# Performance work log

Hardware: AMD Instinct MI355X
Metric: run time of the kernel (lower is better)

The kernel has to match this reference:

```python
import jax, jax.numpy as jnp
import numpy as np

B, T, D, H = 1, 4096, 1024, 16
DK = D // H
SCALE = 1.0 / float(np.sqrt(DK))
NEG = -1e9


def setup_inputs() -> dict:
    key = jax.random.key(0)
    k1, k2, k3 = jax.random.split(key, 3)
    x = jax.random.normal(k1, (B, T, D), dtype=jnp.float32)
    # xavier-ish small weights (gain 0.5)
    Wqkv = jax.random.normal(k2, (3 * D, D), dtype=jnp.float32) * 0.02
    Wout = jax.random.normal(k3, (D, D), dtype=jnp.float32) * 0.02
    return {"x": x, "Wqkv": Wqkv, "Wout": Wout}


def reference(x, Wqkv, Wout):
    b, t, d = x.shape
    # QKV projection (no bias): [B,T,3D] -> [3,B,H,T,DK]
    qkv = jnp.einsum('btd,ed->bte', x, Wqkv)
    qkv = qkv.reshape(b, t, 3, H, DK).transpose(2, 0, 3, 1, 4)
    q, k, v = qkv[0], qkv[1], qkv[2]
    # scaled dot-product scores, clamped
    scores = jnp.einsum('bhtd,bhsd->bhts', q, k) * SCALE
    scores = jnp.clip(scores, -10.0, 10.0)
    # causal additive mask (strict upper triangle gets -1e9)
    mask = jnp.triu(jnp.full((t, t), NEG, dtype=scores.dtype), k=1)
    scores = scores + mask[None, None, :, :]
    attn = jax.nn.softmax(scores, axis=-1)  # dropout is identity in eval
    out = jnp.einsum('bhts,bhsd->bhtd', attn, v)
    out = out.transpose(0, 2, 1, 3).reshape(b, t, d)
    return jnp.einsum('btd,ed->bte', out, Wout)
```

## Files before the change

### kernel.cpp

```cpp
#include <hip/hip_runtime.h>

#define T_SEQ   4096
#define D_MODEL 1024
#define NH      16
#define HD      64
#define E3      3072
#define QSCL    0.125f
#define TILEB   (64L*E3)
#define SLOTSZ  16896
#define P0CAP   800

using u32x2  = __attribute__((ext_vector_type(2))) unsigned int;
using u32x4  = __attribute__((ext_vector_type(4))) unsigned int;
using u16x4  = __attribute__((ext_vector_type(4))) unsigned short;
using u16x8  = __attribute__((ext_vector_type(8))) unsigned short;
using u64x2  = __attribute__((ext_vector_type(2))) unsigned long long;
using f32x4  = __attribute__((ext_vector_type(4))) float;
using bf16x8 = __attribute__((ext_vector_type(8))) __bf16;

__device__ __forceinline__ unsigned short f2bf(float f){
  unsigned int u = __builtin_bit_cast(unsigned int, f);
  u += 0x7fffu + ((u >> 16) & 1u);
  return (unsigned short)(u >> 16);
}
__device__ __forceinline__ float bf2f(unsigned short v){
  unsigned int u = ((unsigned int)v) << 16;
  return __builtin_bit_cast(float, u);
}

__device__ __forceinline__ void gload_lds16(const void* g, void* l){
  __builtin_amdgcn_global_load_lds((const __attribute__((address_space(1))) void*)g,
                                   (__attribute__((address_space(3))) void*)l, 16, 0, 0);
}

__device__ __forceinline__ char* part_ptr(char* p0, char* p1, int slot){
  return (slot < P0CAP) ? p0 + (size_t)slot * SLOTSZ
                        : p1 + (size_t)(slot - P0CAP) * SLOTSZ;
}

#define XN4   (T_SEQ*D_MODEL/4)
#define WQN4  (E3*D_MODEL/4)
#define WON4  (D_MODEL*D_MODEL/4)
__global__ __launch_bounds__(256) void cvt_all(const float4* __restrict__ x,
                                               const float4* __restrict__ wq,
                                               const float4* __restrict__ wo,
                                               u16x4* __restrict__ xb,
                                               u16x4* __restrict__ wqb,
                                               u16x4* __restrict__ wob){
  int i = blockIdx.x * 256 + threadIdx.x;
  const float4* src; u16x4* dst; int j;
  if(i < XN4){ src = x;  dst = xb;  j = i; }
  else if(i < XN4 + WQN4){ src = wq; dst = wqb; j = i - XN4; }
  else { src = wo; dst = wob; j = i - XN4 - WQN4; }
  float4 v = src[j];
  u16x4 o = { f2bf(v.x), f2bf(v.y), f2bf(v.z), f2bf(v.w) };
  dst[j] = o;
}

template<int OUT_BF16, int QSCALE>
__global__ __launch_bounds__(256) void gemm_bt(const unsigned short* __restrict__ A,
                                               const unsigned short* __restrict__ B,
                                               void* __restrict__ Cv,
                                               int M, int N, int K){
  __shared__ unsigned short As[128*32];
  __shared__ unsigned short Bs[128*32];
  const int t    = threadIdx.x;
  const int lane = t & 63;
  const int w    = t >> 6;
  const int brow = blockIdx.y * 128;
  const int bcol = blockIdx.x * 128;
  const int wrow = (w >> 1) * 64;
  const int wcol = (w & 1) * 64;
  const int cc = lane & 15;
  const int gg = lane >> 4;

  f32x4 acc[4][4];
  #pragma unroll
  for(int m=0;m<4;++m)
    #pragma unroll
    for(int n=0;n<4;++n)
      acc[m][n] = (f32x4){0.f,0.f,0.f,0.f};

  const int srow = t >> 2;
  const int sk   = (t & 3) * 8;
  const long aBase = (long)(brow + srow) * K;
  const long bBase = (long)(bcol + srow) * K;

  for(int k0 = 0; k0 < K; k0 += 32){
    __syncthreads();
    gload_lds16(A + aBase + k0 + sk,               As + t*8);
    gload_lds16(A + aBase + 64*(long)K + k0 + sk,  As + 2048 + t*8);
    gload_lds16(B + bBase + k0 + sk,               Bs + t*8);
    gload_lds16(B + bBase + 64*(long)K + k0 + sk,  Bs + 2048 + t*8);
    __syncthreads();

    bf16x8 af[4], bfr[4];
    #pragma unroll
    for(int m=0;m<4;++m)
      af[m]  = *(const bf16x8*)((const char*)As + (wrow + m*16 + cc)*64 + gg*16);
    #pragma unroll
    for(int n=0;n<4;++n)
      bfr[n] = *(const bf16x8*)((const char*)Bs + (wcol + n*16 + cc)*64 + gg*16);
    #pragma unroll
    for(int m=0;m<4;++m)
      #pragma unroll
      for(int n=0;n<4;++n)
        acc[m][n] = __builtin_amdgcn_mfma_f32_16x16x32_bf16(af[m], bfr[n], acc[m][n], 0, 0, 0);
  }

  #pragma unroll
  for(int m=0;m<4;++m){
    #pragma unroll
    for(int n=0;n<4;++n){
      const int row0 = brow + wrow + m*16 + gg*4;
      const int col  = bcol + wcol + n*16 + cc;
      const float sc = (QSCALE && col < D_MODEL) ? QSCL : 1.0f;
      #pragma unroll
      for(int r=0;r<4;++r){
        if constexpr (OUT_BF16 != 0){
          ((unsigned short*)Cv)[(long)(row0 + r)*N + col] = f2bf(acc[m][n][r] * sc);
        } else {
          ((float*)Cv)[(long)(row0 + r)*N + col] = acc[m][n][r];
        }
      }
    }
  }
}

__global__ __launch_bounds__(256) void gemm_bt64(const unsigned short* __restrict__ A,
                                                 const unsigned short* __restrict__ B,
                                                 float* __restrict__ C,
                                                 int M, int N, int K){
  __shared__ unsigned short As[64*32];
  __shared__ unsigned short Bs[128*32];
  const int t    = threadIdx.x;
  const int lane = t & 63;
  const int w    = t >> 6;
  const int brow = blockIdx.y * 64;
  const int bcol = blockIdx.x * 128;
  const int wrow = (w >> 1) * 32;
  const int wcol = (w & 1) * 64;
  const int cc = lane & 15;
  const int gg = lane >> 4;

  f32x4 acc[2][4];
  #pragma unroll
  for(int m=0;m<2;++m)
    #pragma unroll
    for(int n=0;n<4;++n)
      acc[m][n] = (f32x4){0.f,0.f,0.f,0.f};

  const int srow = t >> 2;
  const int sk   = (t & 3) * 8;
  const long aBase = (long)(brow + srow) * K;
  const long bBase = (long)(bcol + srow) * K;

  for(int k0 = 0; k0 < K; k0 += 32){
    __syncthreads();
    gload_lds16(A + aBase + k0 + sk,               As + t*8);
    gload_lds16(B + bBase + k0 + sk,               Bs + t*8);
    gload_lds16(B + bBase + 64*(long)K + k0 + sk,  Bs + 2048 + t*8);
    __syncthreads();

    bf16x8 af[2], bfr[4];
    #pragma unroll
    for(int m=0;m<2;++m)
      af[m]  = *(const bf16x8*)((const char*)As + (wrow + m*16 + cc)*64 + gg*16);
    #pragma unroll
    for(int n=0;n<4;++n)
      bfr[n] = *(const bf16x8*)((const char*)Bs + (wcol + n*16 + cc)*64 + gg*16);
    #pragma unroll
    for(int m=0;m<2;++m)
      #pragma unroll
      for(int n=0;n<4;++n)
        acc[m][n] = __builtin_amdgcn_mfma_f32_16x16x32_bf16(af[m], bfr[n], acc[m][n], 0, 0, 0);
  }

  #pragma unroll
  for(int m=0;m<2;++m){
    #pragma unroll
    for(int n=0;n<4;++n){
      const int row0 = brow + wrow + m*16 + gg*4;
      const int col  = bcol + wcol + n*16 + cc;
      #pragma unroll
      for(int r=0;r<4;++r)
        C[(long)(row0 + r)*N + col] = acc[m][n][r];
    }
  }
}

__global__ __launch_bounds__(256, 3) void attn_part(const unsigned short* __restrict__ qkv,
                                                    unsigned short* __restrict__ attnb,
                                                    char* __restrict__ parts0,
                                                    char* __restrict__ parts1){
  __shared__ char LB[32768];

  const int t    = threadIdx.x;
  const int lane = t & 63;
  const int w    = t >> 6;
  const int cc   = lane & 15;
  const int gg   = lane >> 4;

  const int bid  = blockIdx.x;
  const int hd   = bid & 15;
  const int o_   = bid >> 4;
  const int item = (o_ < 8) ? (7 - o_) : (95 - o_);

  int QB, t0, n, slot;
  if(item < 8){
    QB = item; t0 = 0; n = 2*QB + 2; slot = -1;
  } else if(item < 24){
    const int i = item - 8; QB = 8 + (i >> 1); const int hf = i & 1;
    const int h0 = QB + 1;
    t0 = hf * h0; n = h0;
    slot = (hd*8 + (QB-8))*2 + hf;
  } else {
    const int i = item - 24; QB = 16 + (i >> 2); const int qt = i & 3;
    const int n0 = 2*QB + 2, bsz = n0 >> 2, rem = n0 & 3;
    t0 = qt*bsz + (qt < rem ? qt : rem);
    n  = bsz + (qt < rem ? 1 : 0);
    slot = 256 + (hd*16 + (QB-16))*4 + qt;
  }
  const int gA = 2*QB;
  const int qA = QB*128 + w*16;

  bf16x8 bqA0 = *(const bf16x8*)(qkv + (long)(qA+cc)*E3 + hd*HD +      gg*8);
  bf16x8 bqA1 = *(const bf16x8*)(qkv + (long)(qA+cc)*E3 + hd*HD + 32 + gg*8);
  bf16x8 bqB0 = *(const bf16x8*)(qkv + (long)(qA+64+cc)*E3 + hd*HD +      gg*8);
  bf16x8 bqB1 = *(const bf16x8*)(qkv + (long)(qA+64+cc)*E3 + hd*HD + 32 + gg*8);

  const f32x4 z4 = (f32x4){0.f,0.f,0.f,0.f};
  f32x4 accA0=z4, accA1=z4, accA2=z4, accA3=z4;
  f32x4 accB0=z4, accB1=z4, accB2=z4, accB3=z4;
  float rsA = 0.f, rsB = 0.f;

  const bool lb0 = (4*gg + 0) > cc;
  const bool lb1 = (4*gg + 1) > cc;
  const bool lb2 = (4*gg + 2) > cc;
  const bool lb3 = (4*gg + 3) > cc;

  const int kOffA = cc*128 + (((gg    ) ^ (cc&7)) << 4);
  const int kOffB = cc*128 + (((gg + 4) ^ (cc&7)) << 4);

  const unsigned ldsBase = (unsigned)(unsigned long long)(&LB[0]);
  const unsigned vA0 = ldsBase + 8192  + lane*8;
  const unsigned vA1 = ldsBase + 24576 + lane*8;

  const int kLane0 = (t>>3)*E3 + D_MODEL + hd*HD + (((t&7) ^ ((t>>3)&7)) << 3);
  const int kLane1 = kLane0 + 32*E3;
  const int vLane0 = (4*((t>>3)&15) + ((t&7)>>1))*E3 + 2*D_MODEL + hd*HD
                     + ((2*(t>>7) + (t&1)) << 3);
  const int vLane1 = vLane0 + 32;

  #define STAGE(g_, BUF) do{                                                       \
    const unsigned short* gb_ = qkv + (long)(g_)*TILEB;                            \
    gload_lds16(gb_ + kLane0, LB + (BUF)*16384 + t*16);                            \
    gload_lds16(gb_ + kLane1, LB + (BUF)*16384 + 4096  + t*16);                    \
    gload_lds16(gb_ + vLane0, LB + (BUF)*16384 + 8192  + t*16);                    \
    gload_lds16(gb_ + vLane1, LB + (BUF)*16384 + 12288 + t*16);                    \
  }while(0)

  #define TRRD(d_, va_, OFF_)                                                      \
    asm volatile("ds_read_b64_tr_b16 %0, %1 offset:%c2"                            \
                 : "=v"(d_) : "v"(va_), "i"(OFF_))

  #define PVHALF(vab_, HOFF, doA_, doB_)                                           \
  {                                                                                \
    unsigned long long q0_,q1_,q2_,q3_,q4_,q5_,q6_,q7_;                            \
    TRRD(q0_, vab_, (HOFF) + 0);    TRRD(q1_, vab_, (HOFF) + 512);                 \
    TRRD(q2_, vab_, (HOFF) + 2048); TRRD(q3_, vab_, (HOFF) + 2560);                \
    TRRD(q4_, vab_, (HOFF) + 4096); TRRD(q5_, vab_, (HOFF) + 4608);                \
    TRRD(q6_, vab_, (HOFF) + 6144); TRRD(q7_, vab_, (HOFF) + 6656);                \
    asm volatile("s_waitcnt lgkmcnt(0)");                                          \
    __builtin_amdgcn_sched_barrier(0);                                             \
    u64x2 w0_ = {q0_,q1_}; bf16x8 bv0_ = __builtin_bit_cast(bf16x8, w0_);          \
    u64x2 w1_ = {q2_,q3_}; bf16x8 bv1_ = __builtin_bit_cast(bf16x8, w1_);          \
    u64x2 w2_ = {q4_,q5_}; bf16x8 bv2_ = __builtin_bit_cast(bf16x8, w2_);          \
    u64x2 w3_ = {q6_,q7_}; bf16x8 bv3_ = __builtin_bit_cast(bf16x8, w3_);          \
    if(doA_){                                                                      \
      accA0 = __builtin_amdgcn_mfma_f32_16x16x32_bf16(paA_, bv0_, accA0, 0,0,0);   \
      accA1 = __builtin_amdgcn_mfma_f32_16x16x32_bf16(paA_, bv1_, accA1, 0,0,0);   \
      accA2 = __builtin_amdgcn_mfma_f32_16x16x32_bf16(paA_, bv2_, accA2, 0,0,0);   \
      accA3 = __builtin_amdgcn_mfma_f32_16x16x32_bf16(paA_, bv3_, accA3, 0,0,0);   \
    }                                                                              \
    if(doB_){                                                                      \
      accB0 = __builtin_amdgcn_mfma_f32_16x16x32_bf16(paB_, bv0_, accB0, 0,0,0);   \
      accB1 = __builtin_amdgcn_mfma_f32_16x16x32_bf16(paB_, bv1_, accB1, 0,0,0);   \
      accB2 = __builtin_amdgcn_mfma_f32_16x16x32_bf16(paB_, bv2_, accB2, 0,0,0);   \
      accB3 = __builtin_amdgcn_mfma_f32_16x16x32_bf16(paB_, bv3_, accB3, 0,0,0);   \
    }                                                                              \
  }

  #define PACK4(pk_) (bf16x8){ (__bf16)pk_[0][0],(__bf16)pk_[0][1],(__bf16)pk_[0][2],\
    (__bf16)pk_[0][3],(__bf16)pk_[1][0],(__bf16)pk_[1][1],(__bf16)pk_[1][2],        \
    (__bf16)pk_[1][3] }
  #define PACK4H(pk_) (bf16x8){ (__bf16)pk_[2][0],(__bf16)pk_[2][1],(__bf16)pk_[2][2],\
    (__bf16)pk_[2][3],(__bf16)pk_[3][0],(__bf16)pk_[3][1],(__bf16)pk_[3][2],        \
    (__bf16)pk_[3][3] }

  #define TILE_INT(g_, BUF)                                                        \
  {                                                                                \
    STAGE((g_)+1, (BUF)^1);                                                        \
    const char* kb_ = (const char*)LB + (BUF)*16384;                               \
    float pkA[4][4], pkB[4][4];                                                    \
    _Pragma("unroll")                                                              \
    for(int kt=0; kt<4; ++kt){                                                     \
      bf16x8 a0 = *(const bf16x8*)(kb_ + kOffA + kt*2048);                         \
      bf16x8 a1 = *(const bf16x8*)(kb_ + kOffB + kt*2048);                         \
      f32x4 sA = __builtin_amdgcn_mfma_f32_16x16x32_bf16(a0, bqA0, z4, 0,0,0);     \
      sA = __builtin_amdgcn_mfma_f32_16x16x32_bf16(a1, bqA1, sA, 0,0,0);           \
      f32x4 sB = __builtin_amdgcn_mfma_f32_16x16x32_bf16(a0, bqB0, z4, 0,0,0);     \
      sB = __builtin_amdgcn_mfma_f32_16x16x32_bf16(a1, bqB1, sB, 0,0,0);           \
      _Pragma("unroll")                                                            \
      for(int rr=0; rr<4; ++rr){                                                   \
        float pA_ = __expf(__builtin_amdgcn_fmed3f(sA[rr], -10.f, 10.f));          \
        float pB_ = __expf(__builtin_amdgcn_fmed3f(sB[rr], -10.f, 10.f));          \
        rsA += pA_; rsB += pB_;                                                    \
        pkA[kt][rr] = pA_; pkB[kt][rr] = pB_;                                      \
      }                                                                            \
    }                                                                              \
    bf16x8 paA_, paB_;                                                             \
    const unsigned vab_ = (BUF) ? vA1 : vA0;                                       \
    paA_ = PACK4(pkA);  paB_ = PACK4(pkB);                                         \
    PVHALF(vab_, 0, 1, 1);                                                         \
    paA_ = PACK4H(pkA); paB_ = PACK4H(pkB);                                        \
    PVHALF(vab_, 1024, 1, 1);                                                      \
    __syncthreads();                                                               \
  }

  #define TILE_TAIL(g_, BUFR)                                                      \
  {                                                                                \
    STAGE((g_)+1, (BUFR)^1);                                                       \
    const char* kb_ = (const char*)LB + (BUFR)*16384;                              \
    float pkA[4][4], pkB[4][4];                                                    \
    const bool dA_ = ((g_) == gA);                                                 \
    _Pragma("unroll")                                                              \
    for(int kt=0; kt<4; ++kt){                                                     \
      bf16x8 a0 = *(const bf16x8*)(kb_ + kOffA + kt*2048);                         \
      bf16x8 a1 = *(const bf16x8*)(kb_ + kOffB + kt*2048);                         \
      if(dA_){                                                                     \
        f32x4 sB = __builtin_amdgcn_mfma_f32_16x16x32_bf16(a0, bqB0, z4, 0,0,0);   \
        sB = __builtin_amdgcn_mfma_f32_16x16x32_bf16(a1, bqB1, sB, 0,0,0);         \
        _Pragma("unroll")                                                          \
        for(int rr=0; rr<4; ++rr){                                                 \
          float pB_ = __expf(__builtin_amdgcn_fmed3f(sB[rr], -10.f, 10.f));        \
          rsB += pB_; pkB[kt][rr] = pB_;                                           \
        }                                                                          \
        if(kt <= w){                                                               \
          f32x4 sA = __builtin_amdgcn_mfma_f32_16x16x32_bf16(a0, bqA0, z4, 0,0,0); \
          sA = __builtin_amdgcn_mfma_f32_16x16x32_bf16(a1, bqA1, sA, 0,0,0);       \
          float p0_ = __expf(__builtin_amdgcn_fmed3f(sA[0], -10.f, 10.f));         \
          float p1_ = __expf(__builtin_amdgcn_fmed3f(sA[1], -10.f, 10.f));         \
          float p2_ = __expf(__builtin_amdgcn_fmed3f(sA[2], -10.f, 10.f));         \
          float p3_ = __expf(__builtin_amdgcn_fmed3f(sA[3], -10.f, 10.f));         \
          if(kt == w){                                                             \
            p0_ = lb0 ? 0.f : p0_;  p1_ = lb1 ? 0.f : p1_;                         \
            p2_ = lb2 ? 0.f : p2_;  p3_ = lb3 ? 0.f : p3_;                         \
          }                                                                        \
          rsA += p0_ + p1_ + p2_ + p3_;                                            \
          pkA[kt][0]=p0_; pkA[kt][1]=p1_; pkA[kt][2]=p2_; pkA[kt][3]=p3_;          \
        } else {                                                                   \
          pkA[kt][0]=0.f; pkA[kt][1]=0.f; pkA[kt][2]=0.f; pkA[kt][3]=0.f;          \
        }                                                                          \
      } else {                                                                     \
        pkA[kt][0]=0.f; pkA[kt][1]=0.f; pkA[kt][2]=0.f; pkA[kt][3]=0.f;            \
        if(kt <= w){                                                               \
          f32x4 sB = __builtin_amdgcn_mfma_f32_16x16x32_bf16(a0, bqB0, z4, 0,0,0); \
          sB = __builtin_amdgcn_mfma_f32_16x16x32_bf16(a1, bqB1, sB, 0,0,0);       \
          float p0_ = __expf(__builtin_amdgcn_fmed3f(sB[0], -10.f, 10.f));         \
          float p1_ = __expf(__builtin_amdgcn_fmed3f(sB[1], -10.f, 10.f));         \
          float p2_ = __expf(__builtin_amdgcn_fmed3f(sB[2], -10.f, 10.f));         \
          float p3_ = __expf(__builtin_amdgcn_fmed3f(sB[3], -10.f, 10.f));         \
          if(kt == w){                                                             \
            p0_ = lb0 ? 0.f : p0_;  p1_ = lb1 ? 0.f : p1_;                         \
            p2_ = lb2 ? 0.f : p2_;  p3_ = lb3 ? 0.f : p3_;                         \
          }                                                                        \
          rsB += p0_ + p1_ + p2_ + p3_;                                            \
          pkB[kt][0]=p0_; pkB[kt][1]=p1_; pkB[kt][2]=p2_; pkB[kt][3]=p3_;          \
        } else {                                                                   \
          pkB[kt][0]=0.f; pkB[kt][1]=0.f; pkB[kt][2]=0.f; pkB[kt][3]=0.f;          \
        }                                                                          \
      }                                                                            \
    }                                                                              \
    bf16x8 paA_, paB_;                                                             \
    const unsigned vab_ = (BUFR) ? vA1 : vA0;                                      \
    paA_ = PACK4(pkA);  paB_ = PACK4(pkB);                                         \
    PVHALF(vab_, 0, dA_, 1);                                                       \
    paA_ = PACK4H(pkA); paB_ = PACK4H(pkB);                                        \
    if(w >= 2){ PVHALF(vab_, 1024, dA_, 1); }                                      \
    else if(dA_){ PVHALF(vab_, 1024, 0, 1); }                                      \
    __syncthreads();                                                               \
  }

  STAGE(t0, 0);
  __syncthreads();

  const int gap  = gA - t0;
  const int nInt = (n < gap) ? n : (gap < 0 ? 0 : gap);
  int lt = 0;
  while(lt + 2 <= nInt){
    TILE_INT(t0+lt,   0);
    TILE_INT(t0+lt+1, 1);
    lt += 2;
  }
  if(lt < nInt){ TILE_INT(t0+lt, 0); ++lt; }
  if(lt < n){ TILE_TAIL(t0+lt, (lt&1)); ++lt; }
  if(lt < n){ TILE_TAIL(t0+lt, (lt&1)); ++lt; }

  rsA += __shfl_xor(rsA, 16);  rsA += __shfl_xor(rsA, 32);
  rsB += __shfl_xor(rsB, 16);  rsB += __shfl_xor(rsB, 32);

  if(slot < 0){
    #pragma unroll
    for(int rr=0;rr<4;++rr){
      const float invA = 1.0f / __shfl(rsA, 4*gg + rr);
      const int rowA = qA + 4*gg + rr;
      unsigned short* dA = attnb + (long)rowA*D_MODEL + hd*HD + cc;
      dA[0]  = __builtin_bit_cast(unsigned short, (__bf16)(accA0[rr]*invA));
      dA[16] = __builtin_bit_cast(unsigned short, (__bf16)(accA1[rr]*invA));
      dA[32] = __builtin_bit_cast(unsigned short, (__bf16)(accA2[rr]*invA));
      dA[48] = __builtin_bit_cast(unsigned short, (__bf16)(accA3[rr]*invA));
      const float invB = 1.0f / __shfl(rsB, 4*gg + rr);
      unsigned short* dB = dA + 64L*D_MODEL;
      dB[0]  = __builtin_bit_cast(unsigned short, (__bf16)(accB0[rr]*invB));
      dB[16] = __builtin_bit_cast(unsigned short, (__bf16)(accB1[rr]*invB));
      dB[32] = __builtin_bit_cast(unsigned short, (__bf16)(accB2[rr]*invB));
      dB[48] = __builtin_bit_cast(unsigned short, (__bf16)(accB3[rr]*invB));
    }
  } else {
    char* sp = part_ptr(parts0, parts1, slot);
    #pragma unroll
    for(int rr=0;rr<4;++rr){
      const int rowA = w*16 + 4*gg + rr;
      unsigned short* dA = (unsigned short*)sp + rowA*64 + cc;
      dA[0]  = f2bf(accA0[rr]);
      dA[16] = f2bf(accA1[rr]);
      dA[32] = f2bf(accA2[rr]);
      dA[48] = f2bf(accA3[rr]);
      unsigned short* dB = dA + 64*64;
      dB[0]  = f2bf(accB0[rr]);
      dB[16] = f2bf(accB1[rr]);
      dB[32] = f2bf(accB2[rr]);
      dB[48] = f2bf(accB3[rr]);
    }
    if(gg == 0){
      ((float*)(sp + 16384))[w*16 + cc]      = rsA;
      ((float*)(sp + 16384))[64 + w*16 + cc] = rsB;
    }
  }
  #undef STAGE
  #undef TRRD
  #undef PVHALF
  #undef PACK4
  #undef PACK4H
  #undef TILE_INT
  #undef TILE_TAIL
}

__global__ __launch_bounds__(256) void attn_combine(char* __restrict__ parts0,
                                                    char* __restrict__ parts1,
                                                    unsigned short* __restrict__ attnb){
  const int b  = blockIdx.x;
  const int hd = b & 15;
  const int QB = 8 + (b >> 4);
  const int t  = threadIdx.x;
  const int r  = t >> 1;
  const int d0 = (t & 1) * 32;

  int s0_, np;
  if(QB < 16){ s0_ = (hd*8 + (QB-8))*2;        np = 2; }
  else       { s0_ = 256 + (hd*16 + (QB-16))*4; np = 4; }

  float rs = 0.f;
  float o[32];
  #pragma unroll
  for(int j=0;j<32;++j) o[j] = 0.f;

  for(int pi = 0; pi < np; ++pi){
    const char* pp = part_ptr(parts0, parts1, s0_ + pi);
    rs += ((const float*)(pp + 16384))[r];
    #pragma unroll
    for(int q=0;q<4;++q){
      u16x8 a = *(const u16x8*)(pp + (r*64 + d0 + q*8)*2);
      #pragma unroll
      for(int j=0;j<8;++j) o[q*8+j] += bf2f(a[j]);
    }
  }
  const float inv = 1.0f / rs;
  unsigned short* dst = attnb + (long)(QB*128 + r)*D_MODEL + hd*HD + d0;
  #pragma unroll
  for(int q=0;q<4;++q){
    u16x8 ov;
    #pragma unroll
    for(int j=0;j<8;++j) ov[j] = f2bf(o[q*8+j]*inv);
    *(u16x8*)(dst + q*8) = ov;
  }
}

extern "C" void kernel_launch(void* const* d_in, const int* in_sizes, int n_in,
                              void* d_out, int out_size, void* d_ws, size_t ws_size,
                              hipStream_t stream){
  (void)in_sizes; (void)n_in; (void)out_size; (void)ws_size;
  const float* x    = (const float*)d_in[0];
  const float* wqkv = (const float*)d_in[1];
  const float* wout = (const float*)d_in[2];
  char* ws = (char*)d_ws;
  unsigned short* woutb = (unsigned short*)(ws);
  unsigned short* attnb = (unsigned short*)(ws + (2u  << 20));
  unsigned short* qkvb  = (unsigned short*)(ws + (10u << 20));
  unsigned short* xb    = (unsigned short*)(ws + (34u << 20));
  unsigned short* wqkvb = (unsigned short*)(ws + (42u << 20));
  char*           parts0 = ws + (34u << 20);
  char*           parts1 = (char*)d_out;
  float* out = (float*)d_out;

  cvt_all<<<dim3((XN4 + WQN4 + WON4)/256), 256, 0, stream>>>(
      (const float4*)x, (const float4*)wqkv, (const float4*)wout,
      (u16x4*)xb, (u16x4*)wqkvb, (u16x4*)woutb);

  dim3 g1(E3/128, T_SEQ/128);
  gemm_bt<1,1><<<g1, 256, 0, stream>>>(xb, wqkvb, qkvb, T_SEQ, E3, D_MODEL);

  attn_part<<<dim3(88*NH), 256, 0, stream>>>(qkvb, attnb, parts0, parts1);
  attn_combine<<<dim3(24*NH), 256, 0, stream>>>(parts0, parts1, attnb);

  dim3 g3(D_MODEL/128, T_SEQ/64);
  gemm_bt64<<<g3, 256, 0, stream>>>(attnb, woutb, out, T_SEQ, D_MODEL, D_MODEL);
}
```

Baseline: 122.8 us.

## Deepen QKV GEMM k-tile with swizzled LDS, remap blocks, MFMA row sums

The QKV GEMM now loads 64-wide k-tiles into an XOR-swizzled LDS layout, which halves the barrier count and avoids bank conflicts. It also launches as a 1D grid remapped across 8 groups, likely to spread work across XCDs for L2 locality. The attention kernel computes softmax row sums with an extra MFMA against a ones vector instead of scalar adds and shuffles, and raises its occupancy hint from 3 to 5 waves. The row sums now come from bf16-rounded probabilities, which matches the PV numerator. The trade-offs are more register pressure from the tighter launch bound and one extra MFMA per PV step.

```diff
diff --git a/kernel.cpp b/kernel.cpp
--- a/kernel.cpp
+++ b/kernel.cpp
@@ -62,17 +62,21 @@
                                                const unsigned short* __restrict__ B,
                                                void* __restrict__ Cv,
                                                int M, int N, int K){
-  __shared__ unsigned short As[128*32];
-  __shared__ unsigned short Bs[128*32];
+  __shared__ unsigned short As[128*64];
+  __shared__ unsigned short Bs[128*64];
   const int t    = threadIdx.x;
   const int lane = t & 63;
   const int w    = t >> 6;
-  const int brow = blockIdx.y * 128;
-  const int bcol = blockIdx.x * 128;
+  const int cc   = lane & 15;
+  const int gg   = lane >> 4;
+
+  const int nbx  = N >> 7;
+  const int cpx  = gridDim.x >> 3;
+  const int wg   = (blockIdx.x & 7) * cpx + (blockIdx.x >> 3);
+  const int brow = (wg / nbx) * 128;
+  const int bcol = (wg % nbx) * 128;
   const int wrow = (w >> 1) * 64;
   const int wcol = (w & 1) * 64;
-  const int cc = lane & 15;
-  const int gg = lane >> 4;
 
   f32x4 acc[4][4];
   #pragma unroll
@@ -81,31 +85,39 @@
     for(int n=0;n<4;++n)
       acc[m][n] = (f32x4){0.f,0.f,0.f,0.f};
 
-  const int srow = t >> 2;
-  const int sk   = (t & 3) * 8;
-  const long aBase = (long)(brow + srow) * K;
-  const long bBase = (long)(bcol + srow) * K;
-
-  for(int k0 = 0; k0 < K; k0 += 32){
+  const int  srow = t >> 3;
+  const int  schk = ((t & 7) ^ (srow & 7)) * 8;
+  const long aBase = (long)(brow + srow) * K + schk;
+  const long bBase = (long)(bcol + srow) * K + schk;
+
+  const int kOff0 = cc*128 + (((gg    ) ^ (cc&7)) << 4);
+  const int kOff1 = cc*128 + (((gg + 4) ^ (cc&7)) << 4);
+
+  for(int k0 = 0; k0 < K; k0 += 64){
     __syncthreads();
-    gload_lds16(A + aBase + k0 + sk,               As + t*8);
-    gload_lds16(A + aBase + 64*(long)K + k0 + sk,  As + 2048 + t*8);
-    gload_lds16(B + bBase + k0 + sk,               Bs + t*8);
-    gload_lds16(B + bBase + 64*(long)K + k0 + sk,  Bs + 2048 + t*8);
+    #pragma unroll
+    for(int p=0;p<4;++p){
+      gload_lds16(A + aBase + k0 + (long)p*32*K, (char*)As + p*4096 + t*16);
+      gload_lds16(B + bBase + k0 + (long)p*32*K, (char*)Bs + p*4096 + t*16);
+    }
     __syncthreads();
 
-    bf16x8 af[4], bfr[4];
-    #pragma unroll
-    for(int m=0;m<4;++m)
-      af[m]  = *(const bf16x8*)((const char*)As + (wrow + m*16 + cc)*64 + gg*16);
-    #pragma unroll
-    for(int n=0;n<4;++n)
-      bfr[n] = *(const bf16x8*)((const char*)Bs + (wcol + n*16 + cc)*64 + gg*16);
-    #pragma unroll
-    for(int m=0;m<4;++m)
+    #pragma unroll
+    for(int kk=0;kk<2;++kk){
+      const int off = kk ? kOff1 : kOff0;
+      bf16x8 af[4], bfr[4];
+      #pragma unroll
+      for(int m=0;m<4;++m)
+        af[m]  = *(const bf16x8*)((const char*)As + wrow*128 + m*2048 + off);
       #pragma unroll
       for(int n=0;n<4;++n)
-        acc[m][n] = __builtin_amdgcn_mfma_f32_16x16x32_bf16(af[m], bfr[n], acc[m][n], 0, 0, 0);
+        bfr[n] = *(const bf16x8*)((const char*)Bs + wcol*128 + n*2048 + off);
+      #pragma unroll
+      for(int m=0;m<4;++m)
+        #pragma unroll
+        for(int n=0;n<4;++n)
+          acc[m][n] = __builtin_amdgcn_mfma_f32_16x16x32_bf16(af[m], bfr[n], acc[m][n], 0, 0, 0);
+    }
   }
 
   #pragma unroll
@@ -189,7 +201,7 @@
   }
 }
 
-__global__ __launch_bounds__(256, 3) void attn_part(const unsigned short* __restrict__ qkv,
+__global__ __launch_bounds__(256, 5) void attn_part(const unsigned short* __restrict__ qkv,
                                                     unsigned short* __restrict__ attnb,
                                                     char* __restrict__ parts0,
                                                     char* __restrict__ parts1){
@@ -230,9 +242,11 @@
   bf16x8 bqB1 = *(const bf16x8*)(qkv + (long)(qA+64+cc)*E3 + hd*HD + 32 + gg*8);
 
   const f32x4 z4 = (f32x4){0.f,0.f,0.f,0.f};
-  f32x4 accA0=z4, accA1=z4, accA2=z4, accA3=z4;
-  f32x4 accB0=z4, accB1=z4, accB2=z4, accB3=z4;
-  float rsA = 0.f, rsB = 0.f;
+  const bf16x8 ones = __builtin_bit_cast(bf16x8,
+      (u32x4){0x3F803F80u,0x3F803F80u,0x3F803F80u,0x3F803F80u});
+
+  f32x4 accA0=z4, accA1=z4, accA2=z4, accA3=z4, rsaccA=z4;
+  f32x4 accB0=z4, accB1=z4, accB2=z4, accB3=z4, rsaccB=z4;
 
   const bool lb0 = (4*gg + 0) > cc;
   const bool lb1 = (4*gg + 1) > cc;
@@ -278,12 +292,14 @@
     u64x2 w2_ = {q4_,q5_}; bf16x8 bv2_ = __builtin_bit_cast(bf16x8, w2_);          \
     u64x2 w3_ = {q6_,q7_}; bf16x8 bv3_ = __builtin_bit_cast(bf16x8, w3_);          \
     if(doA_){                                                                      \
+      rsaccA = __builtin_amdgcn_mfma_f32_16x16x32_bf16(paA_, ones, rsaccA, 0,0,0); \
       accA0 = __builtin_amdgcn_mfma_f32_16x16x32_bf16(paA_, bv0_, accA0, 0,0,0);   \
       accA1 = __builtin_amdgcn_mfma_f32_16x16x32_bf16(paA_, bv1_, accA1, 0,0,0);   \
       accA2 = __builtin_amdgcn_mfma_f32_16x16x32_bf16(paA_, bv2_, accA2, 0,0,0);   \
       accA3 = __builtin_amdgcn_mfma_f32_16x16x32_bf16(paA_, bv3_, accA3, 0,0,0);   \
     }                                                                              \
     if(doB_){                                                                      \
+      rsaccB = __builtin_amdgcn_mfma_f32_16x16x32_bf16(paB_, ones, rsaccB, 0,0,0); \
       accB0 = __builtin_amdgcn_mfma_f32_16x16x32_bf16(paB_, bv0_, accB0, 0,0,0);   \
       accB1 = __builtin_amdgcn_mfma_f32_16x16x32_bf16(paB_, bv1_, accB1, 0,0,0);   \
       accB2 = __builtin_amdgcn_mfma_f32_16x16x32_bf16(paB_, bv2_, accB2, 0,0,0);   \
@@ -313,10 +329,8 @@
       sB = __builtin_amdgcn_mfma_f32_16x16x32_bf16(a1, bqB1, sB, 0,0,0);           \
       _Pragma("unroll")                                                            \
       for(int rr=0; rr<4; ++rr){                                                   \
-        float pA_ = __expf(__builtin_amdgcn_fmed3f(sA[rr], -10.f, 10.f));          \
-        float pB_ = __expf(__builtin_amdgcn_fmed3f(sB[rr], -10.f, 10.f));          \
-        rsA += pA_; rsB += pB_;                                                    \
-        pkA[kt][rr] = pA_; pkB[kt][rr] = pB_;                                      \
+        pkA[kt][rr] = __expf(__builtin_amdgcn_fmed3f(sA[rr], -10.f, 10.f));        \
+        pkB[kt][rr] = __expf(__builtin_amdgcn_fmed3f(sB[rr], -10.f, 10.f));        \
       }                                                                            \
     }                                                                              \
     bf16x8 paA_, paB_;                                                             \
@@ -342,10 +356,8 @@
         f32x4 sB = __builtin_amdgcn_mfma_f32_16x16x32_bf16(a0, bqB0, z4, 0,0,0);   \
         sB = __builtin_amdgcn_mfma_f32_16x16x32_bf16(a1, bqB1, sB, 0,0,0);         \
         _Pragma("unroll")                                                          \
-        for(int rr=0; rr<4; ++rr){                                                 \
-          float pB_ = __expf(__builtin_amdgcn_fmed3f(sB[rr], -10.f, 10.f));        \
-          rsB += pB_; pkB[kt][rr] = pB_;                                           \
-        }                                                                          \
+        for(int rr=0; rr<4; ++rr)                                                  \
+          pkB[kt][rr] = __expf(__builtin_amdgcn_fmed3f(sB[rr], -10.f, 10.f));      \
         if(kt <= w){                                                               \
           f32x4 sA = __builtin_amdgcn_mfma_f32_16x16x32_bf16(a0, bqA0, z4, 0,0,0); \
           sA = __builtin_amdgcn_mfma_f32_16x16x32_bf16(a1, bqA1, sA, 0,0,0);       \
@@ -357,7 +369,6 @@
             p0_ = lb0 ? 0.f : p0_;  p1_ = lb1 ? 0.f : p1_;                         \
             p2_ = lb2 ? 0.f : p2_;  p3_ = lb3 ? 0.f : p3_;                         \
           }                                                                        \
-          rsA += p0_ + p1_ + p2_ + p3_;                                            \
           pkA[kt][0]=p0_; pkA[kt][1]=p1_; pkA[kt][2]=p2_; pkA[kt][3]=p3_;          \
         } else {                                                                   \
           pkA[kt][0]=0.f; pkA[kt][1]=0.f; pkA[kt][2]=0.f; pkA[kt][3]=0.f;          \
@@ -375,7 +386,6 @@
             p0_ = lb0 ? 0.f : p0_;  p1_ = lb1 ? 0.f : p1_;                         \
             p2_ = lb2 ? 0.f : p2_;  p3_ = lb3 ? 0.f : p3_;                         \
           }                                                                        \
-          rsB += p0_ + p1_ + p2_ + p3_;                                            \
           pkB[kt][0]=p0_; pkB[kt][1]=p1_; pkB[kt][2]=p2_; pkB[kt][3]=p3_;          \
         } else {                                                                   \
           pkB[kt][0]=0.f; pkB[kt][1]=0.f; pkB[kt][2]=0.f; pkB[kt][3]=0.f;          \
@@ -407,20 +417,17 @@
   if(lt < n){ TILE_TAIL(t0+lt, (lt&1)); ++lt; }
   if(lt < n){ TILE_TAIL(t0+lt, (lt&1)); ++lt; }
 
-  rsA += __shfl_xor(rsA, 16);  rsA += __shfl_xor(rsA, 32);
-  rsB += __shfl_xor(rsB, 16);  rsB += __shfl_xor(rsB, 32);
-
   if(slot < 0){
     #pragma unroll
     for(int rr=0;rr<4;++rr){
-      const float invA = 1.0f / __shfl(rsA, 4*gg + rr);
+      const float invA = 1.0f / rsaccA[rr];
       const int rowA = qA + 4*gg + rr;
       unsigned short* dA = attnb + (long)rowA*D_MODEL + hd*HD + cc;
       dA[0]  = __builtin_bit_cast(unsigned short, (__bf16)(accA0[rr]*invA));
       dA[16] = __builtin_bit_cast(unsigned short, (__bf16)(accA1[rr]*invA));
       dA[32] = __builtin_bit_cast(unsigned short, (__bf16)(accA2[rr]*invA));
       dA[48] = __builtin_bit_cast(unsigned short, (__bf16)(accA3[rr]*invA));
-      const float invB = 1.0f / __shfl(rsB, 4*gg + rr);
+      const float invB = 1.0f / rsaccB[rr];
       unsigned short* dB = dA + 64L*D_MODEL;
       dB[0]  = __builtin_bit_cast(unsigned short, (__bf16)(accB0[rr]*invB));
       dB[16] = __builtin_bit_cast(unsigned short, (__bf16)(accB1[rr]*invB));
@@ -442,10 +449,10 @@
       dB[16] = f2bf(accB1[rr]);
       dB[32] = f2bf(accB2[rr]);
       dB[48] = f2bf(accB3[rr]);
-    }
-    if(gg == 0){
-      ((float*)(sp + 16384))[w*16 + cc]      = rsA;
-      ((float*)(sp + 16384))[64 + w*16 + cc] = rsB;
+      if(cc == 0){
+        ((float*)(sp + 16384))[rowA]      = rsaccA[rr];
+        ((float*)(sp + 16384))[64 + rowA] = rsaccB[rr];
+      }
     }
   }
   #undef STAGE
@@ -518,8 +525,7 @@
       (const float4*)x, (const float4*)wqkv, (const float4*)wout,
       (u16x4*)xb, (u16x4*)wqkvb, (u16x4*)woutb);
 
-  dim3 g1(E3/128, T_SEQ/128);
-  gemm_bt<1,1><<<g1, 256, 0, stream>>>(xb, wqkvb, qkvb, T_SEQ, E3, D_MODEL);
+  gemm_bt<1,1><<<dim3((T_SEQ/128)*(E3/128)), 256, 0, stream>>>(xb, wqkvb, qkvb, T_SEQ, E3, D_MODEL);
 
   attn_part<<<dim3(88*NH), 256, 0, stream>>>(qkvb, attnb, parts0, parts1);
   attn_combine<<<dim3(24*NH), 256, 0, stream>>>(parts0, parts1, attnb);
```

Result: slower. 321.2 us (+161.5%).
